# Kernel tuning notes

Hardware: AMD Instinct MI355X
Metric: run time of the kernel (lower is better)

The kernel has to match this reference:

```python
import jax, jax.numpy as jnp
import numpy as np

TEMPERATURE = 8.0  # sqrt(head_dim=64)
NEG = -1e9


def setup_inputs() -> dict:
    key = jax.random.key(0)
    kq, kk, kv = jax.random.split(key, 3)
    B, H, S, D = 2, 16, 2048, 64
    q = jax.random.normal(kq, (B, H, S, D), dtype=jnp.float32)
    k = jax.random.normal(kk, (B, H, S, D), dtype=jnp.float32)
    v = jax.random.normal(kv, (B, H, S, D), dtype=jnp.float32)
    attn_mask = jnp.ones((B, 1, 1, S), dtype=jnp.int32)  # 1 = keep, 0 = mask
    return {"q": q, "k": k, "v": v, "attn_mask": attn_mask}


def reference(q, k, v, attn_mask):
    # attn = (q / T) @ k^T  -> [B,H,S,S]
    scores = jnp.einsum('bhqd,bhkd->bhqk', q / TEMPERATURE, k)
    # optional padding mask: fill where mask == 0
    scores = jnp.where(attn_mask == 0, NEG, scores)
    # causal mask: triu(diagonal=1) positions are masked (key index > query index)
    S = scores.shape[-1]
    row = jnp.arange(S)[:, None]
    col = jnp.arange(S)[None, :]
    scores = jnp.where(col > row, NEG, scores)
    attn = jax.nn.softmax(scores, axis=-1)
    out = jnp.einsum('bhqk,bhkd->bhqd', attn, v)
    return (out, attn)
```

## Files before the change

### kernel.cpp

```cpp
#include <hip/hip_runtime.h>

#define NEG (-1e9f)

typedef __attribute__((ext_vector_type(8))) short bf16x8;
typedef __attribute__((ext_vector_type(4))) float f32x4;

static constexpr int Ss = 2048, Dd = 64;

__device__ __forceinline__ unsigned short f2bf(float f) {
  union { float f; unsigned u; } v; v.f = f;
  unsigned r = v.u + 0x7FFF + ((v.u >> 16) & 1);
  return (unsigned short)(r >> 16);
}

__global__ __launch_bounds__(256) void attn_kernel(
    const float* __restrict__ q, const float* __restrict__ k,
    const float* __restrict__ v, const int* __restrict__ mask,
    float* __restrict__ out, float* __restrict__ attn) {
  const int tid  = threadIdx.x;
  const int wave = tid >> 6;
  const int lane = tid & 63;
  const int quad = lane >> 4;
  const int ln15 = lane & 15;

  const int bh = blockIdx.x & 31;
  const int qt = 31 - (blockIdx.x >> 5);
  const int b  = bh >> 4;

  __shared__ unsigned short Klds[64 * 72];
  __shared__ unsigned short Vlds[64 * 72];
  __shared__ unsigned short Plds[64 * 72];

  {
    const float* qp = q + ((size_t)bh * Ss + (size_t)qt * 64) * Dd;
#pragma unroll
    for (int i = 0; i < 4; ++i) {
      int idx4 = tid + i * 256;
      int row = idx4 >> 4, col = (idx4 & 15) * 4;
      float4 f = *(const float4*)(qp + row * 64 + col);
      ushort4 u;
      u.x = f2bf(f.x * 0.125f); u.y = f2bf(f.y * 0.125f);
      u.z = f2bf(f.z * 0.125f); u.w = f2bf(f.w * 0.125f);
      *(ushort4*)&Vlds[row * 72 + col] = u;
    }
  }
  __syncthreads();
  const bf16x8 qfrag0 = *(const bf16x8*)&Vlds[(wave * 16 + ln15) * 72 + quad * 8];
  const bf16x8 qfrag1 = *(const bf16x8*)&Vlds[(wave * 16 + ln15) * 72 + quad * 8 + 32];

  float mrow[4], lrow[4];
#pragma unroll
  for (int r = 0; r < 4; ++r) { mrow[r] = -1e30f; lrow[r] = 0.0f; }

  for (int j = 0; j <= qt; ++j) {
    __syncthreads();
    {
      const float* kp = k + ((size_t)bh * Ss + (size_t)j * 64) * Dd;
#pragma unroll
      for (int i = 0; i < 4; ++i) {
        int idx4 = tid + i * 256;
        int row = idx4 >> 4, col = (idx4 & 15) * 4;
        float4 f = *(const float4*)(kp + row * 64 + col);
        ushort4 u;
        u.x = f2bf(f.x); u.y = f2bf(f.y); u.z = f2bf(f.z); u.w = f2bf(f.w);
        *(ushort4*)&Klds[row * 72 + col] = u;
      }
    }
    __syncthreads();
    unsigned long long mm = __ballot(mask[(size_t)b * Ss + j * 64 + lane] != 0);

    float sv[4][4];
#pragma unroll
    for (int c = 0; c < 4; ++c) {
      bf16x8 kf0 = *(const bf16x8*)&Klds[(c * 16 + ln15) * 72 + quad * 8];
      bf16x8 kf1 = *(const bf16x8*)&Klds[(c * 16 + ln15) * 72 + quad * 8 + 32];
      f32x4 acc = {0.f, 0.f, 0.f, 0.f};
      acc = __builtin_amdgcn_mfma_f32_16x16x32_bf16(qfrag0, kf0, acc, 0, 0, 0);
      acc = __builtin_amdgcn_mfma_f32_16x16x32_bf16(qfrag1, kf1, acc, 0, 0, 0);
      int col = j * 64 + c * 16 + ln15;
      bool mz = !((mm >> (c * 16 + ln15)) & 1);
#pragma unroll
      for (int r = 0; r < 4; ++r) {
        int row = qt * 64 + wave * 16 + quad * 4 + r;
        float val = acc[r];
        if (col > row || mz) val = NEG;
        sv[c][r] = val;
      }
    }
#pragma unroll
    for (int r = 0; r < 4; ++r) {
      float tm = fmaxf(fmaxf(sv[0][r], sv[1][r]), fmaxf(sv[2][r], sv[3][r]));
      tm = fmaxf(tm, __shfl_xor(tm, 1));
      tm = fmaxf(tm, __shfl_xor(tm, 2));
      tm = fmaxf(tm, __shfl_xor(tm, 4));
      tm = fmaxf(tm, __shfl_xor(tm, 8));
      float mnew = fmaxf(mrow[r], tm);
      float ss = __expf(sv[0][r] - mnew) + __expf(sv[1][r] - mnew) +
                 __expf(sv[2][r] - mnew) + __expf(sv[3][r] - mnew);
      ss += __shfl_xor(ss, 1);
      ss += __shfl_xor(ss, 2);
      ss += __shfl_xor(ss, 4);
      ss += __shfl_xor(ss, 8);
      lrow[r] = lrow[r] * __expf(mrow[r] - mnew) + ss;
      mrow[r] = mnew;
    }
  }

  float rl[4];
#pragma unroll
  for (int r = 0; r < 4; ++r) rl[r] = 1.0f / lrow[r];

  f32x4 oacc[4];
#pragma unroll
  for (int c = 0; c < 4; ++c) oacc[c] = (f32x4){0.f, 0.f, 0.f, 0.f};

  for (int j = 0; j < 32; ++j) {
    if (j <= qt) {
      __syncthreads();
      {
        const float* kp = k + ((size_t)bh * Ss + (size_t)j * 64) * Dd;
        const float* vp = v + ((size_t)bh * Ss + (size_t)j * 64) * Dd;
#pragma unroll
        for (int i = 0; i < 4; ++i) {
          int idx4 = tid + i * 256;
          int row = idx4 >> 4, col = (idx4 & 15) * 4;
          float4 f = *(const float4*)(kp + row * 64 + col);
          ushort4 u;
          u.x = f2bf(f.x); u.y = f2bf(f.y); u.z = f2bf(f.z); u.w = f2bf(f.w);
          *(ushort4*)&Klds[row * 72 + col] = u;
          float4 g = *(const float4*)(vp + row * 64 + col);
          ushort4 w2;
          w2.x = f2bf(g.x); w2.y = f2bf(g.y); w2.z = f2bf(g.z); w2.w = f2bf(g.w);
          *(ushort4*)&Vlds[row * 72 + col] = w2;
        }
      }
      __syncthreads();
      unsigned long long mm = __ballot(mask[(size_t)b * Ss + j * 64 + lane] != 0);
#pragma unroll
      for (int c = 0; c < 4; ++c) {
        bf16x8 kf0 = *(const bf16x8*)&Klds[(c * 16 + ln15) * 72 + quad * 8];
        bf16x8 kf1 = *(const bf16x8*)&Klds[(c * 16 + ln15) * 72 + quad * 8 + 32];
        f32x4 acc = {0.f, 0.f, 0.f, 0.f};
        acc = __builtin_amdgcn_mfma_f32_16x16x32_bf16(qfrag0, kf0, acc, 0, 0, 0);
        acc = __builtin_amdgcn_mfma_f32_16x16x32_bf16(qfrag1, kf1, acc, 0, 0, 0);
        int col = j * 64 + c * 16 + ln15;
        bool mz = !((mm >> (c * 16 + ln15)) & 1);
#pragma unroll
        for (int r = 0; r < 4; ++r) {
          int row = qt * 64 + wave * 16 + quad * 4 + r;
          float val = acc[r];
          if (col > row || mz) val = NEG;
          float p = __expf(val - mrow[r]) * rl[r];
          attn[((size_t)bh * Ss + row) * Ss + col] = p;
          Plds[(wave * 16 + quad * 4 + r) * 72 + c * 16 + ln15] = f2bf(p);
        }
      }
#pragma unroll
      for (int ch = 0; ch < 2; ++ch) {
        bf16x8 pf = *(const bf16x8*)&Plds[(wave * 16 + ln15) * 72 + quad * 8 + 32 * ch];
#pragma unroll
        for (int c = 0; c < 4; ++c) {
          bf16x8 vf;
#pragma unroll
          for (int jj = 0; jj < 8; ++jj)
            vf[jj] = (short)Vlds[(quad * 8 + jj + 32 * ch) * 72 + c * 16 + ln15];
          oacc[c] = __builtin_amdgcn_mfma_f32_16x16x32_bf16(pf, vf, oacc[c], 0, 0, 0);
        }
      }
    } else {
      float4 z = {0.f, 0.f, 0.f, 0.f};
#pragma unroll
      for (int i = 0; i < 4; ++i) {
        int idx4 = tid + i * 256;
        int row = idx4 >> 4, col = (idx4 & 15) * 4;
        *(float4*)&attn[((size_t)bh * Ss + qt * 64 + row) * Ss + j * 64 + col] = z;
      }
    }
  }

#pragma unroll
  for (int c = 0; c < 4; ++c)
#pragma unroll
    for (int r = 0; r < 4; ++r) {
      int row = qt * 64 + wave * 16 + quad * 4 + r;
      out[((size_t)bh * Ss + row) * Dd + c * 16 + ln15] = oacc[c][r];
    }
}

extern "C" void kernel_launch(void* const* d_in, const int* in_sizes, int n_in,
                              void* d_out, int out_size, void* d_ws, size_t ws_size,
                              hipStream_t stream) {
  const float* q    = (const float*)d_in[0];
  const float* k    = (const float*)d_in[1];
  const float* v    = (const float*)d_in[2];
  const int*   mask = (const int*)d_in[3];
  float* out  = (float*)d_out;
  float* attn = out + (size_t)2 * 16 * 2048 * 64;
  attn_kernel<<<dim3(32 * 32), dim3(256), 0, stream>>>(q, k, v, mask, out, attn);
}
```

Baseline: 698.5 us.

## Pre-convert K/V to bf16 with transposed V and read fragments directly from global

Adds a prep kernel that converts K to bf16 and V to a transposed bf16 layout in workspace. The attention kernel then loads MFMA fragments straight from global memory, with no LDS staging of K/V and no block barriers. It swaps MFMA operand order so each lane owns one query row, which lets it write attn as float4, skip masking on fully unmasked off-diagonal tiles, and store out as vectors. The cost is an extra launch, a workspace round trip, and uncoalesced per-lane global fragment loads; when no workspace is available it falls back to the old kernel.

```diff
diff --git a/kernel.cpp b/kernel.cpp
--- a/kernel.cpp
+++ b/kernel.cpp
@@ -13,7 +13,187 @@
   return (unsigned short)(r >> 16);
 }
 
+__global__ __launch_bounds__(256) void prep_kernel(
+    const float* __restrict__ k, const float* __restrict__ v,
+    unsigned short* __restrict__ kbf, unsigned short* __restrict__ vtbf) {
+  const int tid = threadIdx.x;
+  const int bh = blockIdx.x >> 5;
+  const int st = blockIdx.x & 31;
+  __shared__ unsigned short Vl[64 * 68];
+  const size_t base = ((size_t)bh * Ss + (size_t)st * 64) * Dd;
+#pragma unroll
+  for (int i = 0; i < 4; ++i) {
+    int idx4 = tid + i * 256;
+    int row = idx4 >> 4, col = (idx4 & 15) * 4;
+    float4 f = *(const float4*)(k + base + row * 64 + col);
+    ushort4 u;
+    u.x = f2bf(f.x); u.y = f2bf(f.y); u.z = f2bf(f.z); u.w = f2bf(f.w);
+    *(ushort4*)&kbf[base + row * 64 + col] = u;
+    float4 g = *(const float4*)(v + base + row * 64 + col);
+    ushort4 w;
+    w.x = f2bf(g.x); w.y = f2bf(g.y); w.z = f2bf(g.z); w.w = f2bf(g.w);
+    *(ushort4*)&Vl[row * 68 + col] = w;
+  }
+  __syncthreads();
+  const int d = tid >> 2, sb = (tid & 3) * 16;
+  bf16x8 a, b;
+#pragma unroll
+  for (int i = 0; i < 8; ++i) a[i] = (short)Vl[(sb + i) * 68 + d];
+#pragma unroll
+  for (int i = 0; i < 8; ++i) b[i] = (short)Vl[(sb + 8 + i) * 68 + d];
+  unsigned short* vo = vtbf + ((size_t)bh * Dd + d) * Ss + (size_t)st * 64 + sb;
+  *(bf16x8*)vo = a;
+  *(bf16x8*)(vo + 8) = b;
+}
+
 __global__ __launch_bounds__(256) void attn_kernel(
+    const float* __restrict__ q, const unsigned short* __restrict__ kbf,
+    const unsigned short* __restrict__ vtbf, const int* __restrict__ mask,
+    float* __restrict__ out, float* __restrict__ attn) {
+  const int tid = threadIdx.x;
+  const int wave = tid >> 6, lane = tid & 63, quad = lane >> 4, ln15 = lane & 15;
+  const int bh = blockIdx.x & 31;
+  const int qt = 31 - (blockIdx.x >> 5);
+  const int b = bh >> 4;
+  const int qloc = wave * 16 + ln15;
+  const int qg = qt * 64 + qloc;
+
+  __shared__ unsigned short Plds[64 * 72];
+
+  bf16x8 qf0, qf1;
+  {
+    const float* qp = q + ((size_t)bh * Ss + qg) * Dd + quad * 8;
+    float4 f0 = *(const float4*)(qp);
+    float4 f1 = *(const float4*)(qp + 4);
+    float4 f2 = *(const float4*)(qp + 32);
+    float4 f3 = *(const float4*)(qp + 36);
+    qf0[0] = (short)f2bf(f0.x * 0.125f); qf0[1] = (short)f2bf(f0.y * 0.125f);
+    qf0[2] = (short)f2bf(f0.z * 0.125f); qf0[3] = (short)f2bf(f0.w * 0.125f);
+    qf0[4] = (short)f2bf(f1.x * 0.125f); qf0[5] = (short)f2bf(f1.y * 0.125f);
+    qf0[6] = (short)f2bf(f1.z * 0.125f); qf0[7] = (short)f2bf(f1.w * 0.125f);
+    qf1[0] = (short)f2bf(f2.x * 0.125f); qf1[1] = (short)f2bf(f2.y * 0.125f);
+    qf1[2] = (short)f2bf(f2.z * 0.125f); qf1[3] = (short)f2bf(f2.w * 0.125f);
+    qf1[4] = (short)f2bf(f3.x * 0.125f); qf1[5] = (short)f2bf(f3.y * 0.125f);
+    qf1[6] = (short)f2bf(f3.z * 0.125f); qf1[7] = (short)f2bf(f3.w * 0.125f);
+  }
+
+  const unsigned short* kb = kbf + (size_t)bh * Ss * Dd;
+  const unsigned short* vb = vtbf + (size_t)bh * Dd * Ss;
+  const int* mrowp = mask + (size_t)b * Ss;
+
+  float m = -1e30f, l = 0.0f;
+
+  for (int j = 0; j <= qt; ++j) {
+    unsigned long long mm = __ballot(mrowp[j * 64 + lane] != 0);
+    float sv[16];
+#pragma unroll
+    for (int c = 0; c < 4; ++c) {
+      const unsigned short* kr = kb + (size_t)(j * 64 + c * 16 + ln15) * Dd + quad * 8;
+      bf16x8 kf0 = *(const bf16x8*)(kr);
+      bf16x8 kf1 = *(const bf16x8*)(kr + 32);
+      f32x4 acc = {0.f, 0.f, 0.f, 0.f};
+      acc = __builtin_amdgcn_mfma_f32_16x16x32_bf16(kf0, qf0, acc, 0, 0, 0);
+      acc = __builtin_amdgcn_mfma_f32_16x16x32_bf16(kf1, qf1, acc, 0, 0, 0);
+#pragma unroll
+      for (int r = 0; r < 4; ++r) sv[c * 4 + r] = acc[r];
+    }
+    if (j == qt || mm != ~0ull) {
+#pragma unroll
+      for (int c = 0; c < 4; ++c)
+#pragma unroll
+        for (int r = 0; r < 4; ++r) {
+          int kl = c * 16 + quad * 4 + r;
+          bool mz = !((mm >> kl) & 1);
+          if (j * 64 + kl > qg || mz) sv[c * 4 + r] = NEG;
+        }
+    }
+    float t0 = fmaxf(fmaxf(sv[0], sv[1]), fmaxf(sv[2], sv[3]));
+    float t1 = fmaxf(fmaxf(sv[4], sv[5]), fmaxf(sv[6], sv[7]));
+    float t2 = fmaxf(fmaxf(sv[8], sv[9]), fmaxf(sv[10], sv[11]));
+    float t3 = fmaxf(fmaxf(sv[12], sv[13]), fmaxf(sv[14], sv[15]));
+    float tm = fmaxf(fmaxf(t0, t1), fmaxf(t2, t3));
+    tm = fmaxf(tm, __shfl_xor(tm, 16));
+    tm = fmaxf(tm, __shfl_xor(tm, 32));
+    float mnew = fmaxf(m, tm);
+    float ss = 0.f;
+#pragma unroll
+    for (int i = 0; i < 16; ++i) ss += __expf(sv[i] - mnew);
+    ss += __shfl_xor(ss, 16);
+    ss += __shfl_xor(ss, 32);
+    l = l * __expf(m - mnew) + ss;
+    m = mnew;
+  }
+
+  const float rl = 1.0f / l;
+  f32x4 oacc[4];
+#pragma unroll
+  for (int c = 0; c < 4; ++c) oacc[c] = (f32x4){0.f, 0.f, 0.f, 0.f};
+
+  float* arow = attn + ((size_t)bh * Ss + qg) * Ss;
+
+  for (int j = 0; j < 32; ++j) {
+    if (j <= qt) {
+      unsigned long long mm = __ballot(mrowp[j * 64 + lane] != 0);
+      float sv[16];
+#pragma unroll
+      for (int c = 0; c < 4; ++c) {
+        const unsigned short* kr = kb + (size_t)(j * 64 + c * 16 + ln15) * Dd + quad * 8;
+        bf16x8 kf0 = *(const bf16x8*)(kr);
+        bf16x8 kf1 = *(const bf16x8*)(kr + 32);
+        f32x4 acc = {0.f, 0.f, 0.f, 0.f};
+        acc = __builtin_amdgcn_mfma_f32_16x16x32_bf16(kf0, qf0, acc, 0, 0, 0);
+        acc = __builtin_amdgcn_mfma_f32_16x16x32_bf16(kf1, qf1, acc, 0, 0, 0);
+#pragma unroll
+        for (int r = 0; r < 4; ++r) sv[c * 4 + r] = acc[r];
+      }
+      if (j == qt || mm != ~0ull) {
+#pragma unroll
+        for (int c = 0; c < 4; ++c)
+#pragma unroll
+          for (int r = 0; r < 4; ++r) {
+            int kl = c * 16 + quad * 4 + r;
+            bool mz = !((mm >> kl) & 1);
+            if (j * 64 + kl > qg || mz) sv[c * 4 + r] = NEG;
+          }
+      }
+#pragma unroll
+      for (int c = 0; c < 4; ++c) {
+        float4 pv;
+        pv.x = __expf(sv[c * 4 + 0] - m) * rl;
+        pv.y = __expf(sv[c * 4 + 1] - m) * rl;
+        pv.z = __expf(sv[c * 4 + 2] - m) * rl;
+        pv.w = __expf(sv[c * 4 + 3] - m) * rl;
+        *(float4*)&arow[j * 64 + c * 16 + quad * 4] = pv;
+        ushort4 u;
+        u.x = f2bf(pv.x); u.y = f2bf(pv.y); u.z = f2bf(pv.z); u.w = f2bf(pv.w);
+        *(ushort4*)&Plds[qloc * 72 + c * 16 + quad * 4] = u;
+      }
+#pragma unroll
+      for (int ch = 0; ch < 2; ++ch) {
+        bf16x8 pf = *(const bf16x8*)&Plds[qloc * 72 + quad * 8 + 32 * ch];
+#pragma unroll
+        for (int c = 0; c < 4; ++c) {
+          bf16x8 vf = *(const bf16x8*)&vb[(size_t)(c * 16 + ln15) * Ss + j * 64 + quad * 8 + 32 * ch];
+          oacc[c] = __builtin_amdgcn_mfma_f32_16x16x32_bf16(vf, pf, oacc[c], 0, 0, 0);
+        }
+      }
+    } else {
+      float4 z = {0.f, 0.f, 0.f, 0.f};
+#pragma unroll
+      for (int i = 0; i < 4; ++i) {
+        int idx4 = tid + i * 256;
+        int row = idx4 >> 4, col = (idx4 & 15) * 4;
+        *(float4*)&attn[((size_t)bh * Ss + qt * 64 + row) * Ss + j * 64 + col] = z;
+      }
+    }
+  }
+
+#pragma unroll
+  for (int c = 0; c < 4; ++c)
+    *(f32x4*)&out[((size_t)bh * Ss + qg) * Dd + c * 16 + quad * 4] = oacc[c];
+}
+
+__global__ __launch_bounds__(256) void attn_kernel_fb(
     const float* __restrict__ q, const float* __restrict__ k,
     const float* __restrict__ v, const int* __restrict__ mask,
     float* __restrict__ out, float* __restrict__ attn) {
@@ -106,9 +286,9 @@
     }
   }
 
-  float rl[4];
-#pragma unroll
-  for (int r = 0; r < 4; ++r) rl[r] = 1.0f / lrow[r];
+  float rl4[4];
+#pragma unroll
+  for (int r = 0; r < 4; ++r) rl4[r] = 1.0f / lrow[r];
 
   f32x4 oacc[4];
 #pragma unroll
@@ -150,7 +330,7 @@
           int row = qt * 64 + wave * 16 + quad * 4 + r;
           float val = acc[r];
           if (col > row || mz) val = NEG;
-          float p = __expf(val - mrow[r]) * rl[r];
+          float p = __expf(val - mrow[r]) * rl4[r];
           attn[((size_t)bh * Ss + row) * Ss + col] = p;
           Plds[(wave * 16 + quad * 4 + r) * 72 + c * 16 + ln15] = f2bf(p);
         }
@@ -196,5 +376,14 @@
   const int*   mask = (const int*)d_in[3];
   float* out  = (float*)d_out;
   float* attn = out + (size_t)2 * 16 * 2048 * 64;
-  attn_kernel<<<dim3(32 * 32), dim3(256), 0, stream>>>(q, k, v, mask, out, attn);
-}
+
+  const size_t need = (size_t)2 * 32 * Ss * Dd * sizeof(unsigned short);
+  if (d_ws != nullptr && ws_size >= need) {
+    unsigned short* kbf  = (unsigned short*)d_ws;
+    unsigned short* vtbf = kbf + (size_t)32 * Ss * Dd;
+    prep_kernel<<<dim3(32 * 32), dim3(256), 0, stream>>>(k, v, kbf, vtbf);
+    attn_kernel<<<dim3(32 * 32), dim3(256), 0, stream>>>(q, kbf, vtbf, mask, out, attn);
+  } else {
+    attn_kernel_fb<<<dim3(32 * 32), dim3(256), 0, stream>>>(q, k, v, mask, out, attn);
+  }
+}
```

New measurement: 769.3 us. +10.1%, slower.
